# Performance work log

Hardware: AMD Instinct MI355X
Metric: run time of the kernel (lower is better)

The kernel has to match this reference:

```python
import jax, jax.numpy as jnp
import numpy as np

BS = 256          # batch size
N = 1000          # n_step_per_batch
ORDER = 2         # derivative order -> 3 vars (u, u', u'') per step
D = ORDER + 1
STEP_LOGIT = float(np.log(0.001 / 0.999))  # logit(0.001); sigmoid -> 0.001 step size


def mlp(x, w1, b1, w2, b2, w3, b3):
    h = jax.nn.relu(x @ w1 + b1)
    h = jax.nn.relu(h @ w2 + b2)
    return h @ w3 + b3


def build_A(c, h):
    # c: (N, 3) per-step equation coefficients; h: (N-1,) step sizes.
    # Rows: [1 initial-value] + [N equation] + [2*(N-1) Taylor smoothness (d=0,1)].
    R = 1 + N + 2 * (N - 1)
    i = jnp.arange(N)
    j = jnp.arange(N - 1)
    ones = jnp.ones(N - 1, c.dtype)
    rows = jnp.concatenate([
        jnp.array([0]),
        jnp.repeat(1 + i, 3),
        jnp.repeat(1 + N + 2 * j, 4),
        jnp.repeat(2 + N + 2 * j, 3)])
    cols = jnp.concatenate([
        jnp.array([0]),
        (i[:, None] * 3 + jnp.arange(3)).ravel(),
        jnp.stack([3 * j, 3 * j + 1, 3 * j + 2, 3 * (j + 1)], axis=1).ravel(),
        jnp.stack([3 * j + 1, 3 * j + 2, 3 * j + 4], axis=1).ravel()])
    vals = jnp.concatenate([
        jnp.ones(1, c.dtype),
        c.ravel(),
        jnp.stack([-ones, -h, -h * h / 2, ones], axis=1).ravel(),
        jnp.stack([-ones, -h, ones], axis=1).ravel()])
    return jnp.zeros((R, 3 * N), c.dtype).at[rows, cols].add(vals)


def ode_solve(coeffs, rhs, init_iv, steps):
    # coeffs (bs,1,N,3), rhs (bs,N,1), init_iv (bs,1), steps (bs,1,N-1)
    # coeffs/steps are batch-uniform in this model -> single shared system matrix.
    c = coeffs[0, 0]
    h = steps[0, 0]
    A = build_A(c, h)                       # (R, 3N)
    R = A.shape[0]
    b = jnp.zeros((R, BS), A.dtype)
    b = b.at[0].set(init_iv[:, 0]).at[1:1 + N].set(rhs[:, :, 0].T)
    AtA = A.T @ A + 1e-8 * jnp.eye(3 * N, dtype=A.dtype)
    u = jnp.linalg.solve(AtA, A.T @ b)      # (3N, BS) least-squares trajectory
    resid = A @ u - b
    eps = jnp.sqrt(jnp.sum(resid * resid, axis=0))  # (BS,) equation slack norm
    u = u.reshape(N, 3, BS)
    x0 = u[:, 0].T[:, :, None]              # (bs, N, 1)
    x1 = u[:, 1].T[:, :, None]
    x2 = u[:, 2].T[:, :, None]
    return x0, x1, x2, eps, steps


def reference(pin, ptime, pw1, pb1, pw2, pb2, pw3, pb3,
              tw1, tb1, tw2, tb2, tw3, tb3,
              nw1, nb1, nw2, nb2, nw3, nb3, net_iv):
    xi = mlp(pin, pw1, pb1, pw2, pb2, pw3, pb3).reshape(1, 3)
    ts = mlp(ptime, tw1, tb1, tw2, tb2, tw3, tb3).reshape(1, N)
    xi = jnp.tile(xi, (BS, 1))
    ts = jnp.tile(ts, (BS, 1))
    alpha = xi[:, 0:1][:, None, :]                 # (bs,1,1)
    beta = xi[:, 1:2][:, None, :]
    powr = jax.nn.sigmoid(xi[:, 2:3][:, None, :])
    ts = ts[:, None, :]                            # (bs,1,N)
    var = mlp(net_iv.reshape(BS, -1), nw1, nb1, nw2, nb2, nw3, nb3).reshape(BS, 1, N)
    rhs = jnp.abs(alpha * ts + beta * ts ** 2) ** powr * var ** 2 + ts
    rhs = jnp.transpose(rhs, (0, 2, 1))            # (bs, N, 1)
    coeffs = jnp.broadcast_to(jnp.array([0.0, 1.0, 0.0], net_iv.dtype), (BS, 1, N, 3))
    init_iv = var[:, :, 0]                         # (bs, 1)
    steps = jax.nn.sigmoid(jnp.full((BS, 1, N - 1), STEP_LOGIT, net_iv.dtype))
    x0, x1, x2, eps, steps = ode_solve(coeffs, rhs, init_iv, steps)
    x0 = jnp.transpose(x0, (0, 2, 1))              # (bs, 1, N)
    var = jnp.transpose(var, (0, 2, 1))            # (bs, N, 1)
    return (x0, steps, eps, var, ts[:, 0, :], alpha, beta, powr)


def setup_inputs() -> dict:
    key = jax.random.key(0)
    ks = jax.random.split(key, 24)
    f32 = jnp.float32

    def w(k, shape, scale=0.03):
        return (scale * jax.random.normal(k, shape)).astype(f32)

    inp = {
        "pin": w(ks[0], (1, 64), 1.0),
        "ptime": w(ks[1], (1, 64), 1.0),
        "pw1": w(ks[2], (64, 1024)), "pb1": jnp.zeros((1024,), f32),
        "pw2": w(ks[3], (1024, 1024)), "pb2": jnp.zeros((1024,), f32),
        "pw3": w(ks[4], (1024, 3)), "pb3": jnp.zeros((3,), f32),
        "tw1": w(ks[5], (64, 1024)), "tb1": jnp.zeros((1024,), f32),
        "tw2": w(ks[6], (1024, 1024)), "tb2": jnp.zeros((1024,), f32),
        "tw3": w(ks[7], (1024, N)), "tb3": jnp.zeros((N,), f32),
        "nw1": w(ks[8], (N, 1024)), "nb1": jnp.zeros((1024,), f32),
        "nw2": w(ks[9], (1024, 1024)), "nb2": jnp.zeros((1024,), f32),
        "nw3": w(ks[10], (1024, N)), "nb3": jnp.zeros((N,), f32),
        "net_iv": jax.random.normal(ks[11], (BS, N)).astype(f32),
    }
    return inp
```

## Files before the change

### kernel.cpp

```cpp
#include <hip/hip_runtime.h>
#include <math.h>

#define NN 1000
#define NIT 4
#define NKT 16

typedef _Float16 f16;
typedef _Float16 f16x8 __attribute__((ext_vector_type(8)));
typedef _Float16 f16x4 __attribute__((ext_vector_type(4)));
typedef float    f32x4 __attribute__((ext_vector_type(4)));

#define WS_H1P 0
#define WS_H1T 1024
#define WS_H2P 2048
#define WS_H2T 3072
#define WS_TS  4096
#define WS_XI  5120
#define WF_A0  540672
#define WF_H1  802816
#define WF_H2  1064960
#define WF_BT1 1327104
#define WF_BT2 2375680
#define WF_BT3 3424256

#define O_X0    0
#define O_STEP  256000
#define O_EPS   511744
#define O_VAR   512000
#define O_TS    768000
#define O_ALPHA 1024000
#define O_BETA  1024256
#define O_POWR  1024512

__device__ __forceinline__ void conv_bt_body(int idx, const float* __restrict__ W, int K0, int NW,
                                             f16* __restrict__ BT, float (*T)[32][33])
{
    const int tid = threadIdx.x;
    const int tx = tid & 31, ty = tid >> 5;
    const int kt = (idx & 31) * 32, ntile = (idx >> 5) * 32;
    #pragma unroll
    for (int i = 0; i < 4; ++i) {
        int k = kt + ty + i * 8, n = ntile + tx;
        (*T)[ty + i * 8][tx] = (k < K0 && n < NW) ? W[(size_t)k * NW + n] : 0.f;
    }
    __syncthreads();
    #pragma unroll
    for (int i = 0; i < 4; ++i) {
        int n = ntile + ty + i * 8, k = kt + tx;
        BT[(size_t)n * 1024 + k] = (f16)(*T)[tx][ty + i * 8];
    }
}

__device__ __forceinline__ void conv_a_body(int row, const float* __restrict__ in, f16* __restrict__ a0)
{
    const int t = threadIdx.x;
    float4 v = {0.f, 0.f, 0.f, 0.f};
    if (t < 250) v = ((const float4*)(in + row * 1000))[t];
    f16x4 h = {(f16)v.x, (f16)v.y, (f16)v.z, (f16)v.w};
    *(f16x4*)&a0[row * 1024 + t * 4] = h;
}

__device__ __forceinline__ void l1_body(int sub, const float* __restrict__ pin,
    const float* __restrict__ pw1, const float* __restrict__ pb1,
    const float* __restrict__ ptime, const float* __restrict__ tw1, const float* __restrict__ tb1,
    float* __restrict__ ws, float* sin_)
{
    const int tid = threadIdx.x;
    const bool tp = sub >= 4;
    const float* in = tp ? ptime : pin;
    const float* W  = tp ? tw1 : pw1;
    const float* B  = tp ? tb1 : pb1;
    float* outp = ws + (tp ? WS_H1T : WS_H1P);
    const int bxl = sub & 3;
    if (tid < 64) sin_[tid] = in[tid];
    __syncthreads();
    const int u = bxl * 256 + tid;
    float acc = B[u];
    #pragma unroll 16
    for (int k = 0; k < 64; ++k) acc += sin_[k] * W[k * 1024 + u];
    outp[u] = fmaxf(acc, 0.f);
}

__device__ __forceinline__ void l2_body(int lb, const float* __restrict__ pw2, const float* __restrict__ pb2,
    const float* __restrict__ tw2, const float* __restrict__ tb2, float* __restrict__ ws,
    float (*red)[16][17])
{
    const bool tp = lb >= 64;
    const float* h = ws + (tp ? WS_H1T : WS_H1P);
    const float* W = tp ? tw2 : pw2;
    const float* B = tp ? tb2 : pb2;
    float* outp = ws + (tp ? WS_H2T : WS_H2P);
    const int u0 = (lb & 63) * 16;
    const int tid = threadIdx.x, ul = tid & 15, kc = tid >> 4;
    const float* wp = W + u0 + ul;
    float acc = 0.f;
    const int kbase = kc * 64;
    #pragma unroll 8
    for (int k = 0; k < 64; ++k) acc += h[kbase + k] * wp[(size_t)(kbase + k) * 1024];
    (*red)[kc][ul] = acc; __syncthreads();
    for (int s = 8; s; s >>= 1) { if (kc < s) (*red)[kc][ul] += (*red)[kc + s][ul]; __syncthreads(); }
    if (tid < 16) outp[u0 + tid] = fmaxf((*red)[0][tid] + B[u0 + tid], 0.f);
}

__device__ __forceinline__ void l3_body(int lb, const float* __restrict__ pw3, const float* __restrict__ pb3,
    const float* __restrict__ tw3, const float* __restrict__ tb3,
    float* __restrict__ ws, float* __restrict__ out,
    float (*red)[16][17], float* redx)
{
    const int tid = threadIdx.x;
    if (lb == 64) {
        const float* h2p = ws + WS_H2P;
        float p[3] = {0.f, 0.f, 0.f};
        for (int k = tid; k < 1024; k += 256) {
            float h = h2p[k];
            p[0] += h * pw3[k * 3 + 0];
            p[1] += h * pw3[k * 3 + 1];
            p[2] += h * pw3[k * 3 + 2];
        }
        float xi[3];
        #pragma unroll
        for (int j = 0; j < 3; ++j) {
            redx[tid] = p[j]; __syncthreads();
            for (int s = 128; s > 0; s >>= 1) {
                if (tid < s) redx[tid] += redx[tid + s];
                __syncthreads();
            }
            xi[j] = redx[0] + pb3[j];
            __syncthreads();
        }
        float alpha = xi[0], beta = xi[1];
        float powr = 1.f / (1.f + expf(-xi[2]));
        if (tid == 0) { ws[WS_XI + 0] = alpha; ws[WS_XI + 1] = beta; ws[WS_XI + 2] = powr; }
        out[O_ALPHA + tid] = alpha;
        out[O_BETA  + tid] = beta;
        out[O_POWR  + tid] = powr;
    } else {
        const float* h = ws + WS_H2T;
        const int u0 = lb * 16;
        const int ul = tid & 15, kc = tid >> 4;
        const int u = u0 + ul;
        float acc = 0.f;
        const int kbase = kc * 64;
        if (u < NN) {
            #pragma unroll 8
            for (int k = 0; k < 64; ++k) acc += h[kbase + k] * tw3[(size_t)(kbase + k) * NN + u];
        }
        (*red)[kc][ul] = acc; __syncthreads();
        for (int s = 8; s; s >>= 1) { if (kc < s) (*red)[kc][ul] += (*red)[kc + s][ul]; __syncthreads(); }
        if (tid < 16 && u0 + tid < NN) ws[WS_TS + u0 + tid] = (*red)[0][tid] + tb3[u0 + tid];
    }
}

template<bool F16OUT>
__device__ __forceinline__ void gemm16_body(int bx, const f16* __restrict__ A, const f16* __restrict__ BT,
    const float* __restrict__ bias, int NW, f16* __restrict__ Cf16, float* __restrict__ Cf32, int ldc,
    f16 (*As)[32][72], f16 (*Bs)[32][72])
{
    const int tid = threadIdx.x;
    const int lane = tid & 63, wave = tid >> 6;
    const int wm = wave >> 1, wn = wave & 1;
    const int m0 = (bx >> 5) * 32, n0 = (bx & 31) * 32;
    const int srow = tid >> 3, sc = tid & 7;
    const float4* gA = (const float4*)(A  + (size_t)(m0 + srow) * 1024 + sc * 8);
    const float4* gB = (const float4*)(BT + (size_t)(n0 + srow) * 1024 + sc * 8);

    f32x4 acc = {0.f, 0.f, 0.f, 0.f};

    float4 ra = gA[0], rb = gB[0];
    *(float4*)&As[0][srow][sc * 8] = ra;
    *(float4*)&Bs[0][srow][sc * 8] = rb;
    ra = gA[8]; rb = gB[8];
    __syncthreads();

    const int arow = wm * 16 + (lane & 15);
    const int brow = wn * 16 + (lane & 15);
    const int kf = (lane >> 4) * 8;

    #pragma unroll 2
    for (int t = 0; t < NKT; ++t) {
        const int cur = t & 1;
        float4 ra2 = {}, rb2 = {};
        if (t + 2 < NKT) { ra2 = gA[(t + 2) * 8]; rb2 = gB[(t + 2) * 8]; }

        const f16x8 a0 = *(const f16x8*)&As[cur][arow][kf];
        const f16x8 b0 = *(const f16x8*)&Bs[cur][brow][kf];
        acc = __builtin_amdgcn_mfma_f32_16x16x32_f16(a0, b0, acc, 0, 0, 0);
        const f16x8 a1 = *(const f16x8*)&As[cur][arow][32 + kf];
        const f16x8 b1 = *(const f16x8*)&Bs[cur][brow][32 + kf];
        acc = __builtin_amdgcn_mfma_f32_16x16x32_f16(a1, b1, acc, 0, 0, 0);

        __syncthreads();
        if (t + 1 < NKT) {
            *(float4*)&As[cur ^ 1][srow][sc * 8] = ra;
            *(float4*)&Bs[cur ^ 1][srow][sc * 8] = rb;
        }
        ra = ra2; rb = rb2;
        __syncthreads();
    }

    const int col = n0 + wn * 16 + (lane & 15);
    const int row = m0 + wm * 16 + (lane >> 4) * 4;
    const float bs = (col < NW) ? bias[col] : 0.f;
    #pragma unroll
    for (int j = 0; j < 4; ++j) {
        float v = acc[j] + bs;
        if (F16OUT) {
            v = fmaxf(v, 0.f);
            Cf16[(size_t)(row + j) * 1024 + col] = (f16)v;
        } else if (col < NW) {
            Cf32[(size_t)(row + j) * ldc + col] = v;
        }
    }
}

__global__ __launch_bounds__(256) void k_s1(const float* __restrict__ nw1, const float* __restrict__ net_iv,
    const float* __restrict__ pin, const float* __restrict__ pw1, const float* __restrict__ pb1,
    const float* __restrict__ ptime, const float* __restrict__ tw1, const float* __restrict__ tb1,
    float* __restrict__ ws, f16* __restrict__ wsh)
{
    __shared__ float T[32][33];
    __shared__ float sin_[64];
    const int bx = blockIdx.x;
    if (bx < 1024) {
        conv_bt_body(bx, nw1, 1000, 1024, wsh + WF_BT1, &T);
    } else if (bx < 1280) {
        conv_a_body(bx - 1024, net_iv, wsh + WF_A0);
    } else {
        l1_body(bx - 1280, pin, pw1, pb1, ptime, tw1, tb1, ws, sin_);
    }
}

__global__ __launch_bounds__(256) void k_s2(const float* __restrict__ nw2, const float* __restrict__ nb1,
    const float* __restrict__ pw2, const float* __restrict__ pb2,
    const float* __restrict__ tw2, const float* __restrict__ tb2,
    float* __restrict__ ws, f16* __restrict__ wsh)
{
    __shared__ f16 As[2][32][72];
    __shared__ f16 Bs[2][32][72];
    __shared__ float T[32][33];
    __shared__ float red[16][17];
    const int bx = blockIdx.x;
    if (bx < 256) {
        gemm16_body<true>(bx, wsh + WF_A0, wsh + WF_BT1, nb1, 1024, wsh + WF_H1, nullptr, 0, As, Bs);
    } else if (bx < 1280) {
        conv_bt_body(bx - 256, nw2, 1024, 1024, wsh + WF_BT2, &T);
    } else {
        l2_body(bx - 1280, pw2, pb2, tw2, tb2, ws, &red);
    }
}

__global__ __launch_bounds__(256) void k_s3(const float* __restrict__ nw3, const float* __restrict__ nb2,
    const float* __restrict__ pw3, const float* __restrict__ pb3,
    const float* __restrict__ tw3, const float* __restrict__ tb3,
    float* __restrict__ ws, f16* __restrict__ wsh, float* __restrict__ out)
{
    __shared__ f16 As[2][32][72];
    __shared__ f16 Bs[2][32][72];
    __shared__ float T[32][33];
    __shared__ float red[16][17];
    __shared__ float redx[256];
    const int bx = blockIdx.x;
    if (bx < 256) {
        gemm16_body<true>(bx, wsh + WF_H1, wsh + WF_BT2, nb2, 1024, wsh + WF_H2, nullptr, 0, As, Bs);
    } else if (bx < 1280) {
        conv_bt_body(bx - 256, nw3, 1024, 1000, wsh + WF_BT3, &T);
    } else {
        l3_body(bx - 1280, pw3, pb3, tw3, tb3, ws, out, &red, redx);
    }
}

__global__ __launch_bounds__(256) void k_s4(const float* __restrict__ nb3,
    f16* __restrict__ wsh, float* __restrict__ out)
{
    __shared__ f16 As[2][32][72];
    __shared__ f16 Bs[2][32][72];
    gemm16_body<false>(blockIdx.x, wsh + WF_H2, wsh + WF_BT3, nb3, 1000,
                       nullptr, out + O_VAR, 1000, As, Bs);
}

__device__ inline void d_shift_left(const double a[4], double b4[4], double* sh, int tid, double pad)
{
    __syncthreads();
    sh[tid] = a[0];
    __syncthreads();
    b4[0] = a[1]; b4[1] = a[2]; b4[2] = a[3];
    b4[3] = (tid < 255) ? sh[tid + 1] : pad;
}
__device__ inline void d_scan_fwd(const double a[4], double incl[4], double* swt, int tid)
{
    double p0 = a[0], p1 = p0 + a[1], p2 = p1 + a[2], p3 = p2 + a[3];
    int lane = tid & 63, wid = tid >> 6;
    double w = p3;
    #pragma unroll
    for (int d = 1; d < 64; d <<= 1) {
        double t = __shfl_up(w, d, 64);
        if (lane >= d) w += t;
    }
    __syncthreads();
    if (lane == 63) swt[wid] = w;
    __syncthreads();
    double off = w - p3;
    #pragma unroll
    for (int q = 0; q < 3; ++q) if (q < wid) off += swt[q];
    incl[0] = p0 + off; incl[1] = p1 + off; incl[2] = p2 + off; incl[3] = p3 + off;
}
__device__ inline void d_scan_rev(const double a[4], double incl[4], double* swt, int tid)
{
    double s3 = a[3], s2 = s3 + a[2], s1 = s2 + a[1], s0 = s1 + a[0];
    int lane = tid & 63, wid = tid >> 6;
    double w = s0;
    #pragma unroll
    for (int d = 1; d < 64; d <<= 1) {
        double t = __shfl_down(w, d, 64);
        if (lane < 64 - d) w += t;
    }
    __syncthreads();
    if (lane == 0) swt[wid] = w;
    __syncthreads();
    double off = w - s0;
    #pragma unroll
    for (int q = 1; q < 4; ++q) if (q > wid) off += swt[q];
    incl[0] = s0 + off; incl[1] = s1 + off; incl[2] = s2 + off; incl[3] = s3 + off;
}

__global__ __launch_bounds__(256) void k_ode(const float* __restrict__ ws, float* __restrict__ out)
{
    const int b = blockIdx.x;
    const int tid = threadIdx.x;
    const double H = 0.001, H2c = 0.5e-6, INVH = 1000.0, EPSR = 1e-8;

    __shared__ double sh[257];
    __shared__ double swt[4];

    const float alpha = ws[WS_XI + 0], beta = ws[WS_XI + 1], powr = ws[WS_XI + 2];

    const float4 tsv = *(const float4*)&ws[WS_TS + tid * 4];
    const float* varp = out + O_VAR + (size_t)b * NN;
    float vaa[4];
    #pragma unroll
    for (int k = 0; k < 4; ++k) {
        int i = tid * 4 + k;
        vaa[k] = (i < NN) ? varp[i] : 0.f;
    }
    const double init = (double)varp[0];

    float tsa[4] = {tsv.x, tsv.y, tsv.z, tsv.w};

    double r[4];
    #pragma unroll
    for (int k = 0; k < 4; ++k) {
        int i = tid * 4 + k;
        float tf = tsa[k], vf = vaa[k];
        float basef = fabsf(alpha * tf + beta * tf * tf);
        float rr = powf(basef, powr) * vf * vf + tf;
        r[k] = (i < NN) ? (double)rr : 0.0;
    }

    double rn[4];
    d_shift_left(r, rn, sh, tid, 0.0);
    double ux[4], ud[4], us[4], g[4], gi[4];
    #pragma unroll
    for (int k = 0; k < 4; ++k) {
        int i = tid * 4 + k;
        ud[k] = r[k];
        us[k] = (i < NN - 1) ? (rn[k] - r[k]) * INVH : 0.0;
        g[k]  = (i < NN - 1) ? 0.5 * H * (r[k] + rn[k]) : 0.0;
    }
    d_scan_fwd(g, gi, swt, tid);
    #pragma unroll
    for (int k = 0; k < 4; ++k) {
        int i = tid * 4 + k;
        ux[k] = (i < NN) ? (init + (gi[k] - g[k])) : 0.0;
    }

    double tx[4] = {0,0,0,0}, td[4] = {0,0,0,0}, tss[4] = {0,0,0,0};
    for (int it = 0; it < NIT; ++it) {
        double a[4], yx0 = 0.0;
        #pragma unroll
        for (int k = 0; k < 4; ++k) {
            int i = tid * 4 + k;
            double yx = ux[k] - EPSR * tx[k];
            if (k == 0) yx0 = yx;
            a[k] = (i == 0) ? 0.0 : yx;
        }
        double S[4]; d_scan_rev(a, S, swt, tid);
        double wP[4];
        #pragma unroll
        for (int k = 0; k < 4; ++k) wP[k] = S[k] - a[k];
        double wV[4];
        #pragma unroll
        for (int k = 0; k < 4; ++k) {
            int i = tid * 4 + k;
            double ys = us[k] - EPSR * tss[k];
            wV[k] = (i < NN - 1) ? -(ys + H2c * wP[k]) * INVH : 0.0;
        }
        __syncthreads();
        sh[tid] = wV[3];
        if (tid == 0) sh[256] = yx0 + wP[0];
        __syncthreads();
        double wVm[4];
        wVm[1] = wV[0]; wVm[2] = wV[1]; wVm[3] = wV[2];
        wVm[0] = (tid > 0) ? sh[tid - 1] : 0.0;
        const double w0 = sh[256];

        double wD[4];
        #pragma unroll
        for (int k = 0; k < 4; ++k) {
            int i = tid * 4 + k;
            double yd = ud[k] - EPSR * td[k];
            wD[k] = (i < NN) ? (yd + ((i < NN - 1) ? H * wP[k] : 0.0) - wVm[k] + wV[k]) : 0.0;
        }
        double wDn[4]; d_shift_left(wD, wDn, sh, tid, 0.0);
        #pragma unroll
        for (int k = 0; k < 4; ++k) {
            int i = tid * 4 + k;
            td[k]  = wD[k];
            tss[k] = (i < NN - 1) ? (wDn[k] - wD[k] - wV[k]) * INVH : 0.0;
            g[k]   = (i < NN - 1) ? (H * td[k] + H2c * tss[k] + wP[k]) : 0.0;
        }
        d_scan_fwd(g, gi, swt, tid);
        #pragma unroll
        for (int k = 0; k < 4; ++k) {
            int i = tid * 4 + k;
            tx[k] = (i < NN) ? (w0 + (gi[k] - g[k])) : 0.0;
        }
    }

    double dx[4], dd[4], ds_[4];
    #pragma unroll
    for (int k = 0; k < 4; ++k) { dx[k] = -EPSR * tx[k]; dd[k] = -EPSR * td[k]; ds_[k] = -EPSR * tss[k]; }

    #pragma unroll
    for (int k = 0; k < 4; ++k) {
        int i = tid * 4 + k;
        if (i < NN) {
            out[O_X0  + b * NN + i] = (float)(ux[k] + dx[k]);
            out[O_TS  + b * NN + i] = tsa[k];
        }
        if (i < NN - 1) out[O_STEP + b * (NN - 1) + i] = 0.001f;
    }

    double dxn[4], ddn[4];
    d_shift_left(dx, dxn, sh, tid, 0.0);
    d_shift_left(dd, ddn, sh, tid, 0.0);
    double ss = 0.0;
    #pragma unroll
    for (int k = 0; k < 4; ++k) {
        int i = tid * 4 + k;
        if (i < NN) ss += dd[k] * dd[k];
        if (i == 0) ss += dx[k] * dx[k];
        if (i < NN - 1) {
            double rp = dxn[k] - dx[k] - H * dd[k] - H2c * ds_[k];
            double rv = ddn[k] - dd[k] - H * ds_[k];
            ss += rp * rp + rv * rv;
        }
    }
    const int lane = tid & 63, wid = tid >> 6;
    #pragma unroll
    for (int d = 32; d; d >>= 1) ss += __shfl_down(ss, d, 64);
    __syncthreads();
    if (lane == 0) swt[wid] = ss;
    __syncthreads();
    if (tid == 0) out[O_EPS + b] = (float)sqrt(swt[0] + swt[1] + swt[2] + swt[3]);
}

extern "C" void kernel_launch(void* const* d_in, const int* in_sizes, int n_in,
                              void* d_out, int out_size, void* d_ws, size_t ws_size,
                              hipStream_t stream)
{
    const float* pin    = (const float*)d_in[0];
    const float* ptime  = (const float*)d_in[1];
    const float* pw1    = (const float*)d_in[2];
    const float* pb1    = (const float*)d_in[3];
    const float* pw2    = (const float*)d_in[4];
    const float* pb2    = (const float*)d_in[5];
    const float* pw3    = (const float*)d_in[6];
    const float* pb3    = (const float*)d_in[7];
    const float* tw1    = (const float*)d_in[8];
    const float* tb1    = (const float*)d_in[9];
    const float* tw2    = (const float*)d_in[10];
    const float* tb2    = (const float*)d_in[11];
    const float* tw3    = (const float*)d_in[12];
    const float* tb3    = (const float*)d_in[13];
    const float* nw1    = (const float*)d_in[14];
    const float* nb1    = (const float*)d_in[15];
    const float* nw2    = (const float*)d_in[16];
    const float* nb2    = (const float*)d_in[17];
    const float* nw3    = (const float*)d_in[18];
    const float* nb3    = (const float*)d_in[19];
    const float* net_iv = (const float*)d_in[20];
    float* out = (float*)d_out;
    float* ws  = (float*)d_ws;
    f16*   wsh = (f16*)d_ws;

    k_s1 <<<1288, 256, 0, stream>>>(nw1, net_iv, pin, pw1, pb1, ptime, tw1, tb1, ws, wsh);
    k_s2 <<<1408, 256, 0, stream>>>(nw2, nb1, pw2, pb2, tw2, tb2, ws, wsh);
    k_s3 <<<1345, 256, 0, stream>>>(nw3, nb2, pw3, pb3, tw3, tb3, ws, wsh, out);
    k_s4 <<<256,  256, 0, stream>>>(nb3, wsh, out);
    k_ode<<<256,  256, 0, stream>>>(ws, out);
}
```

Measured before the change: 44.19 us.

## Fuse fp32-to-fp16 conversion into first GEMM and drop one launch

The first network layer GEMM now reads fp32 activations and fp32 weights directly, converting them to fp16 while staging into shared memory. This removes the separate conversion passes for net_iv and nw1 and their workspace round-trip. The later weight conversions and GEMMs are each shifted one stage earlier, which removes the fourth launch. The cost is an uncoalesced-ish transposed store of B into LDS and wider fp32 global loads inside the GEMM loop.

```diff
diff --git a/kernel.cpp b/kernel.cpp
--- a/kernel.cpp
+++ b/kernel.cpp
@@ -7,7 +7,7 @@
 
 typedef _Float16 f16;
 typedef _Float16 f16x8 __attribute__((ext_vector_type(8)));
-typedef _Float16 f16x4 __attribute__((ext_vector_type(4)));
+typedef _Float16 f16x2 __attribute__((ext_vector_type(2)));
 typedef float    f32x4 __attribute__((ext_vector_type(4)));
 
 #define WS_H1P 0
@@ -16,10 +16,8 @@
 #define WS_H2T 3072
 #define WS_TS  4096
 #define WS_XI  5120
-#define WF_A0  540672
 #define WF_H1  802816
 #define WF_H2  1064960
-#define WF_BT1 1327104
 #define WF_BT2 2375680
 #define WF_BT3 3424256
 
@@ -49,15 +47,6 @@
         int n = ntile + ty + i * 8, k = kt + tx;
         BT[(size_t)n * 1024 + k] = (f16)(*T)[tx][ty + i * 8];
     }
-}
-
-__device__ __forceinline__ void conv_a_body(int row, const float* __restrict__ in, f16* __restrict__ a0)
-{
-    const int t = threadIdx.x;
-    float4 v = {0.f, 0.f, 0.f, 0.f};
-    if (t < 250) v = ((const float4*)(in + row * 1000))[t];
-    f16x4 h = {(f16)v.x, (f16)v.y, (f16)v.z, (f16)v.w};
-    *(f16x4*)&a0[row * 1024 + t * 4] = h;
 }
 
 __device__ __forceinline__ void l1_body(int sub, const float* __restrict__ pin,
@@ -151,6 +140,96 @@
     }
 }
 
+__device__ __forceinline__ void gemm_conv_body(int bx,
+    const float* __restrict__ Af, int ldA, int K0,
+    const float* __restrict__ W, int NW, const float* __restrict__ bias,
+    f16* __restrict__ Cf16,
+    f16 (*As)[32][72], f16 (*Bs)[32][72])
+{
+    const int tid = threadIdx.x;
+    const int lane = tid & 63, wave = tid >> 6;
+    const int wm = wave >> 1, wn = wave & 1;
+    const int m0 = (bx >> 5) * 32, n0b = (bx & 31) * 32;
+
+    const int sarow = tid >> 3, sac = (tid & 7) * 8;
+    const int sbk = (tid >> 3) * 2, sbn = (tid & 7) * 4;
+    const int bcol_ok = (n0b + sbn) < NW;
+
+    f16x8 pa; float4 pb0, pb1;
+
+    auto loadA = [&](int k0, f16x8& o) {
+        float4 x = {0.f,0.f,0.f,0.f}, y = {0.f,0.f,0.f,0.f};
+        if (k0 + sac < K0) {
+            const float* p = Af + (size_t)(m0 + sarow) * ldA + k0 + sac;
+            x = *(const float4*)p;
+            y = *(const float4*)(p + 4);
+        }
+        f16x8 h = {(f16)x.x,(f16)x.y,(f16)x.z,(f16)x.w,
+                   (f16)y.x,(f16)y.y,(f16)y.z,(f16)y.w};
+        o = h;
+    };
+    auto loadB = [&](int k0, float4& b0, float4& b1) {
+        b0 = {0.f,0.f,0.f,0.f}; b1 = {0.f,0.f,0.f,0.f};
+        const int r0 = k0 + sbk;
+        if (bcol_ok) {
+            const float* p = W + (size_t)r0 * NW + n0b + sbn;
+            if (r0 < K0)     b0 = *(const float4*)p;
+            if (r0 + 1 < K0) b1 = *(const float4*)(p + NW);
+        }
+    };
+    auto storeA = [&](int buf, const f16x8& v) {
+        *(f16x8*)&As[buf][sarow][sac] = v;
+    };
+    auto storeB = [&](int buf, const float4& b0, const float4& b1) {
+        f16x2 v0 = {(f16)b0.x, (f16)b1.x}; *(f16x2*)&Bs[buf][sbn + 0][sbk] = v0;
+        f16x2 v1 = {(f16)b0.y, (f16)b1.y}; *(f16x2*)&Bs[buf][sbn + 1][sbk] = v1;
+        f16x2 v2 = {(f16)b0.z, (f16)b1.z}; *(f16x2*)&Bs[buf][sbn + 2][sbk] = v2;
+        f16x2 v3 = {(f16)b0.w, (f16)b1.w}; *(f16x2*)&Bs[buf][sbn + 3][sbk] = v3;
+    };
+
+    f32x4 acc = {0.f, 0.f, 0.f, 0.f};
+
+    loadA(0, pa); loadB(0, pb0, pb1);
+    storeA(0, pa); storeB(0, pb0, pb1);
+    loadA(64, pa); loadB(64, pb0, pb1);
+    __syncthreads();
+
+    const int arow = wm * 16 + (lane & 15);
+    const int brow = wn * 16 + (lane & 15);
+    const int kf = (lane >> 4) * 8;
+
+    #pragma unroll 2
+    for (int t = 0; t < NKT; ++t) {
+        const int cur = t & 1;
+        f16x8 na; float4 nb0 = {}, nb1 = {};
+        if (t + 2 < NKT) { loadA((t + 2) * 64, na); loadB((t + 2) * 64, nb0, nb1); }
+
+        const f16x8 a0 = *(const f16x8*)&As[cur][arow][kf];
+        const f16x8 b0 = *(const f16x8*)&Bs[cur][brow][kf];
+        acc = __builtin_amdgcn_mfma_f32_16x16x32_f16(a0, b0, acc, 0, 0, 0);
+        const f16x8 a1 = *(const f16x8*)&As[cur][arow][32 + kf];
+        const f16x8 b1 = *(const f16x8*)&Bs[cur][brow][32 + kf];
+        acc = __builtin_amdgcn_mfma_f32_16x16x32_f16(a1, b1, acc, 0, 0, 0);
+
+        __syncthreads();
+        if (t + 1 < NKT) {
+            storeA(cur ^ 1, pa);
+            storeB(cur ^ 1, pb0, pb1);
+        }
+        pa = na; pb0 = nb0; pb1 = nb1;
+        __syncthreads();
+    }
+
+    const int col = n0b + wn * 16 + (lane & 15);
+    const int row = m0 + wm * 16 + (lane >> 4) * 4;
+    const float bs = (col < NW) ? bias[col] : 0.f;
+    #pragma unroll
+    for (int j = 0; j < 4; ++j) {
+        float v = fmaxf(acc[j] + bs, 0.f);
+        Cf16[(size_t)(row + j) * 1024 + col] = (f16)v;
+    }
+}
+
 template<bool F16OUT>
 __device__ __forceinline__ void gemm16_body(int bx, const f16* __restrict__ A, const f16* __restrict__ BT,
     const float* __restrict__ bias, int NW, f16* __restrict__ Cf16, float* __restrict__ Cf32, int ldc,
@@ -213,24 +292,27 @@
     }
 }
 
-__global__ __launch_bounds__(256) void k_s1(const float* __restrict__ nw1, const float* __restrict__ net_iv,
+__global__ __launch_bounds__(256) void k_s1(const float* __restrict__ net_iv,
+    const float* __restrict__ nw1, const float* __restrict__ nb1, const float* __restrict__ nw2,
     const float* __restrict__ pin, const float* __restrict__ pw1, const float* __restrict__ pb1,
     const float* __restrict__ ptime, const float* __restrict__ tw1, const float* __restrict__ tb1,
     float* __restrict__ ws, f16* __restrict__ wsh)
 {
+    __shared__ f16 As[2][32][72];
+    __shared__ f16 Bs[2][32][72];
     __shared__ float T[32][33];
     __shared__ float sin_[64];
     const int bx = blockIdx.x;
-    if (bx < 1024) {
-        conv_bt_body(bx, nw1, 1000, 1024, wsh + WF_BT1, &T);
-    } else if (bx < 1280) {
-        conv_a_body(bx - 1024, net_iv, wsh + WF_A0);
+    if (bx < 256) {
+        gemm_conv_body(bx, net_iv, 1000, 1000, nw1, 1024, nb1, wsh + WF_H1, As, Bs);
+    } else if (bx < 264) {
+        l1_body(bx - 256, pin, pw1, pb1, ptime, tw1, tb1, ws, sin_);
     } else {
-        l1_body(bx - 1280, pin, pw1, pb1, ptime, tw1, tb1, ws, sin_);
-    }
-}
-
-__global__ __launch_bounds__(256) void k_s2(const float* __restrict__ nw2, const float* __restrict__ nb1,
+        conv_bt_body(bx - 264, nw2, 1024, 1024, wsh + WF_BT2, &T);
+    }
+}
+
+__global__ __launch_bounds__(256) void k_s2(const float* __restrict__ nw3, const float* __restrict__ nb2,
     const float* __restrict__ pw2, const float* __restrict__ pb2,
     const float* __restrict__ tw2, const float* __restrict__ tb2,
     float* __restrict__ ws, f16* __restrict__ wsh)
@@ -241,41 +323,30 @@
     __shared__ float red[16][17];
     const int bx = blockIdx.x;
     if (bx < 256) {
-        gemm16_body<true>(bx, wsh + WF_A0, wsh + WF_BT1, nb1, 1024, wsh + WF_H1, nullptr, 0, As, Bs);
+        gemm16_body<true>(bx, wsh + WF_H1, wsh + WF_BT2, nb2, 1024, wsh + WF_H2, nullptr, 0, As, Bs);
     } else if (bx < 1280) {
-        conv_bt_body(bx - 256, nw2, 1024, 1024, wsh + WF_BT2, &T);
+        conv_bt_body(bx - 256, nw3, 1024, 1000, wsh + WF_BT3, &T);
     } else {
         l2_body(bx - 1280, pw2, pb2, tw2, tb2, ws, &red);
     }
 }
 
-__global__ __launch_bounds__(256) void k_s3(const float* __restrict__ nw3, const float* __restrict__ nb2,
+__global__ __launch_bounds__(256) void k_s3(const float* __restrict__ nb3,
     const float* __restrict__ pw3, const float* __restrict__ pb3,
     const float* __restrict__ tw3, const float* __restrict__ tb3,
     float* __restrict__ ws, f16* __restrict__ wsh, float* __restrict__ out)
 {
     __shared__ f16 As[2][32][72];
     __shared__ f16 Bs[2][32][72];
-    __shared__ float T[32][33];
     __shared__ float red[16][17];
     __shared__ float redx[256];
     const int bx = blockIdx.x;
     if (bx < 256) {
-        gemm16_body<true>(bx, wsh + WF_H1, wsh + WF_BT2, nb2, 1024, wsh + WF_H2, nullptr, 0, As, Bs);
-    } else if (bx < 1280) {
-        conv_bt_body(bx - 256, nw3, 1024, 1000, wsh + WF_BT3, &T);
+        gemm16_body<false>(bx, wsh + WF_H2, wsh + WF_BT3, nb3, 1000,
+                           nullptr, out + O_VAR, 1000, As, Bs);
     } else {
-        l3_body(bx - 1280, pw3, pb3, tw3, tb3, ws, out, &red, redx);
-    }
-}
-
-__global__ __launch_bounds__(256) void k_s4(const float* __restrict__ nb3,
-    f16* __restrict__ wsh, float* __restrict__ out)
-{
-    __shared__ f16 As[2][32][72];
-    __shared__ f16 Bs[2][32][72];
-    gemm16_body<false>(blockIdx.x, wsh + WF_H2, wsh + WF_BT3, nb3, 1000,
-                       nullptr, out + O_VAR, 1000, As, Bs);
+        l3_body(bx - 256, pw3, pb3, tw3, tb3, ws, out, &red, redx);
+    }
 }
 
 __device__ inline void d_shift_left(const double a[4], double b4[4], double* sh, int tid, double pad)
@@ -493,9 +564,8 @@
     float* ws  = (float*)d_ws;
     f16*   wsh = (f16*)d_ws;
 
-    k_s1 <<<1288, 256, 0, stream>>>(nw1, net_iv, pin, pw1, pb1, ptime, tw1, tb1, ws, wsh);
-    k_s2 <<<1408, 256, 0, stream>>>(nw2, nb1, pw2, pb2, tw2, tb2, ws, wsh);
-    k_s3 <<<1345, 256, 0, stream>>>(nw3, nb2, pw3, pb3, tw3, tb3, ws, wsh, out);
-    k_s4 <<<256,  256, 0, stream>>>(nb3, wsh, out);
+    k_s1 <<<1288, 256, 0, stream>>>(net_iv, nw1, nb1, nw2, pin, pw1, pb1, ptime, tw1, tb1, ws, wsh);
+    k_s2 <<<1408, 256, 0, stream>>>(nw3, nb2, pw2, pb2, tw2, tb2, ws, wsh);
+    k_s3 <<<321,  256, 0, stream>>>(nb3, pw3, pb3, tw3, tb3, ws, wsh, out);
     k_ode<<<256,  256, 0, stream>>>(ws, out);
 }
```

Result: slower. 45.31 us (+2.5%).
